# Kernel optimization log

Hardware: AMD Instinct MI355X
Metric: run time of the kernel (lower is better)

Reference implementation:

```python
import jax, jax.numpy as jnp
import numpy as np

B, T, C, H = 2, 2048, 1024, 16
HD = C // H  # head dim = 64


def setup_inputs() -> dict:
    key = jax.random.key(0)
    ks = jax.random.split(key, 5)
    s = 0.02
    return {
        "x": jax.random.normal(ks[0], (B, T, C), dtype=jnp.float32),
        "w_attn": jax.random.normal(ks[1], (C, 3 * C), dtype=jnp.float32) * s,
        "b_attn": jnp.zeros((3 * C,), dtype=jnp.float32),
        "w_proj": jax.random.normal(ks[2], (C, C), dtype=jnp.float32) * s,
        "b_proj": jnp.zeros((C,), dtype=jnp.float32),
    }


def reference(x, w_attn, b_attn, w_proj, b_proj):
    Bc, Tc, Cc = x.shape
    qkv = x @ w_attn + b_attn                      # [B,T,3C]
    q, k, v = jnp.split(qkv, 3, axis=2)            # each [B,T,C]
    # [B,T,C] -> [B,H,T,HD]
    def heads(t):
        return t.reshape(Bc, Tc, H, HD).transpose(0, 2, 1, 3)
    q, k, v = heads(q), heads(k), heads(v)
    scale = 1.0 / jnp.sqrt(jnp.asarray(HD, dtype=x.dtype))
    att = jnp.einsum("bhqd,bhkd->bhqk", q, k) * scale   # [B,H,T,T]
    causal = jnp.tril(jnp.ones((Tc, Tc), dtype=bool))
    att = jnp.where(causal, att, jnp.asarray(-jnp.inf, dtype=att.dtype))
    att = jax.nn.softmax(att, axis=-1)
    y = jnp.einsum("bhqk,bhkd->bhqd", att, v)            # [B,H,T,HD]
    y = y.transpose(0, 2, 1, 3).reshape(Bc, Tc, Cc)      # [B,T,C]
    return y @ w_proj + b_proj
```

## Files before the change

### kernel.cpp

```cpp
#include <hip/hip_runtime.h>
#include <stdint.h>


typedef short bf16x8 __attribute__((ext_vector_type(8)));
typedef float f32x4 __attribute__((ext_vector_type(4)));

__device__ inline unsigned short f2bf(float f) {
  union { float f; uint32_t u; } v; v.f = f;
  uint32_t u = v.u;
  u += 0x7FFFu + ((u >> 16) & 1u);
  return (unsigned short)(u >> 16);
}

__device__ inline unsigned pkbf(float a, float b) {
  unsigned r;
  asm("v_cvt_pk_bf16_f32 %0, %1, %2" : "=v"(r) : "v"(a), "v"(b));
  return r;
}

__device__ inline float exp2_fast(float x) {
#if __has_builtin(__builtin_amdgcn_exp2f)
  return __builtin_amdgcn_exp2f(x);
#else
  float r; asm("v_exp_f32 %0, %1" : "=v"(r) : "v"(x)); return r;
#endif
}

__device__ inline void load_lds16(const unsigned short* g, unsigned short* l) {
  __builtin_amdgcn_global_load_lds(
      (const __attribute__((address_space(1))) unsigned int*)(const void*)g,
      (__attribute__((address_space(3))) unsigned int*)(void*)l, 16, 0, 0);
}

__global__ __launch_bounds__(256) void cast_bf16_kernel(
    const float* __restrict__ in, unsigned short* __restrict__ out, int n4) {
  int i = blockIdx.x * 256 + threadIdx.x;
  if (i >= n4) return;
  float4 f = reinterpret_cast<const float4*>(in)[i];
  ushort4 o;
  o.x = f2bf(f.x); o.y = f2bf(f.y); o.z = f2bf(f.z); o.w = f2bf(f.w);
  reinterpret_cast<ushort4*>(out)[i] = o;
}

__global__ void transpose_cast_kernel(
    const float* __restrict__ in, unsigned short* __restrict__ out, int R, int Cn) {
  __shared__ float tile[32][33];
  int bx = blockIdx.x * 32, by = blockIdx.y * 32;
  int tx = threadIdx.x, ty = threadIdx.y;
  #pragma unroll
  for (int i = 0; i < 32; i += 8)
    tile[ty + i][tx] = in[(size_t)(by + ty + i) * Cn + bx + tx];
  __syncthreads();
  #pragma unroll
  for (int i = 0; i < 32; i += 8)
    out[(size_t)(bx + ty + i) * R + by + tx] = f2bf(tile[tx][ty + i]);
}

template<int BM, int BN>
__global__ __launch_bounds__(256) void gemm_bt_kernel(
    const unsigned short* __restrict__ A,
    const unsigned short* __restrict__ Bt,
    const float* __restrict__ bias,
    void* __restrict__ outp,
    unsigned short* __restrict__ vtp,
    int M, int N, int K, int mode) {
  constexpr int MT = BM / 32, NT = BN / 32;
  constexpr int RPWA = BM / 4, RPWB = BN / 4;
  constexpr int NJA = RPWA / 16, NJB = RPWB / 16;
  __shared__ unsigned short As[2][BM * 32];
  __shared__ unsigned short Bs[2][BN * 32];
  const int t = threadIdx.x;
  const int wave = t >> 6, lane = t & 63;
  const int L = lane & 15, quad = lane >> 4;
  const int wm = (wave >> 1) * (BM / 2), wn = (wave & 1) * (BN / 2);
  const int m0 = blockIdx.y * BM, n0 = blockIdx.x * BN;

  const int drow = lane >> 2;
  const int dch  = (lane & 3) ^ ((drow >> 1) & 3);
  const int foff = ((quad ^ ((L >> 1) & 3)) * 8);

  const unsigned short* Ab = A  + (size_t)(m0 + wave * RPWA + drow) * K + dch * 8;
  const unsigned short* Bb = Bt + (size_t)(n0 + wave * RPWB + drow) * K + dch * 8;

  f32x4 acc[MT][NT] = {};
  const int NK = K >> 5;

  #pragma unroll
  for (int j = 0; j < NJA; ++j)
    load_lds16(Ab + (size_t)j * 16 * K, &As[0][(wave * RPWA + j * 16) * 32]);
  #pragma unroll
  for (int j = 0; j < NJB; ++j)
    load_lds16(Bb + (size_t)j * 16 * K, &Bs[0][(wave * RPWB + j * 16) * 32]);

  int buf = 0;
  for (int kt = 0; kt < NK; ++kt) {
    asm volatile("" ::: "memory");
    __builtin_amdgcn_s_waitcnt(0x0F70);
    __builtin_amdgcn_s_barrier();
    asm volatile("" ::: "memory");

    if (kt + 1 < NK) {
      #pragma unroll
      for (int j = 0; j < NJA; ++j)
        load_lds16(Ab + (size_t)j * 16 * K + (kt + 1) * 32,
                   &As[buf ^ 1][(wave * RPWA + j * 16) * 32]);
      #pragma unroll
      for (int j = 0; j < NJB; ++j)
        load_lds16(Bb + (size_t)j * 16 * K + (kt + 1) * 32,
                   &Bs[buf ^ 1][(wave * RPWB + j * 16) * 32]);
    }

    bf16x8 af[MT], bf[NT];
    #pragma unroll
    for (int mt = 0; mt < MT; ++mt)
      af[mt] = *reinterpret_cast<const bf16x8*>(&As[buf][(wm + mt * 16 + L) * 32 + foff]);
    #pragma unroll
    for (int nt = 0; nt < NT; ++nt)
      bf[nt] = *reinterpret_cast<const bf16x8*>(&Bs[buf][(wn + nt * 16 + L) * 32 + foff]);
    __builtin_amdgcn_s_setprio(1);
    #pragma unroll
    for (int mt = 0; mt < MT; ++mt)
      #pragma unroll
      for (int nt = 0; nt < NT; ++nt)
        acc[mt][nt] = __builtin_amdgcn_mfma_f32_16x16x32_bf16(af[mt], bf[nt], acc[mt][nt], 0, 0, 0);
    __builtin_amdgcn_s_setprio(0);
    buf ^= 1;
  }

  if (mode == 0) {
    float* out = (float*)outp;
    #pragma unroll
    for (int mt = 0; mt < MT; ++mt)
      #pragma unroll
      for (int nt = 0; nt < NT; ++nt) {
        int col = n0 + wn + nt * 16 + L;
        float b = bias[col];
        #pragma unroll
        for (int r = 0; r < 4; ++r) {
          int row = m0 + wm + mt * 16 + quad * 4 + r;
          out[(size_t)row * N + col] = acc[mt][nt][r] + b;
        }
      }
  } else {
    unsigned short* qkv = (unsigned short*)outp;
    #pragma unroll
    for (int mt = 0; mt < MT; ++mt)
      #pragma unroll
      for (int nt = 0; nt < NT; ++nt) {
        int col = n0 + wn + nt * 16 + L;
        int sel = col >> 10, cc = col & 1023;
        int h = cc >> 6, d = cc & 63;
        float b = bias[col];
        float sc = (sel == 0) ? 0.18033688011112042f : 1.0f;
        #pragma unroll
        for (int r = 0; r < 4; ++r) {
          int row = m0 + wm + mt * 16 + quad * 4 + r;
          int bb = row >> 11, tt = row & 2047;
          float val = (acc[mt][nt][r] + b) * sc;
          if (sel == 2) {
            vtp[((size_t)(bb * 16 + h) * 64 + d) * 2048 + tt] = f2bf(val);
          } else {
            qkv[(((size_t)sel * 32 + (size_t)(bb * 16 + h)) * 2048 + tt) * 64 + d] = f2bf(val);
          }
        }
      }
  }
}

__global__ __launch_bounds__(256) void attn_kernel(
    const unsigned short* __restrict__ qkv,
    const unsigned short* __restrict__ vt,
    unsigned short* __restrict__ y) {
  __shared__ unsigned short Ks[3][64 * 64];
  __shared__ unsigned short Vs[3][64 * 64];
  __shared__ unsigned short Ps[4][32][72];

  const int t = threadIdx.x;
  const int wave = t >> 6, lane = t & 63;
  const int L = lane & 15, quad = lane >> 4;
  const int b = blockIdx.x;
  const int bh = (b & 7) * 4 + ((b >> 3) & 3);
  const int pi = b >> 5;
  const int tA = pi, tB = 31 - pi;
  const int rowA0 = tA * 64 + wave * 16;
  const int rowB0 = tB * 64 + wave * 16;
  const int ntiles = tB + 1;

  const unsigned short* qb  = qkv + ((size_t)bh * 2048) * 64;
  const unsigned short* kb  = qkv + ((size_t)(32 + bh) * 2048) * 64;
  const unsigned short* vtb = vt + (size_t)bh * 64 * 2048;

  const int drow = lane >> 3;
  const int dch  = (lane & 7) ^ drow;
  const int fo0 = ((quad ^ (L & 7)) * 8);
  const int fo1 = (((quad + 4) ^ (L & 7)) * 8);

  bf16x8 qfA[2], qfB[2];
  #pragma unroll
  for (int h = 0; h < 2; ++h) {
    qfA[h] = *reinterpret_cast<const bf16x8*>(qb + (size_t)(rowA0 + L) * 64 + h * 32 + quad * 8);
    qfB[h] = *reinterpret_cast<const bf16x8*>(qb + (size_t)(rowB0 + L) * 64 + h * 32 + quad * 8);
  }

  f32x4 oA[4] = {}, oB[4] = {};
  float rsA = 0.f, rsB = 0.f;

  {
    #pragma unroll
    for (int j = 0; j < 2; ++j) {
      int r0 = wave * 16 + j * 8;
      load_lds16(kb  + (size_t)(0 + r0 + drow) * 64 + dch * 8, &Ks[0][r0 * 64]);
      load_lds16(vtb + (size_t)(r0 + drow) * 2048 + 0 + dch * 8, &Vs[0][r0 * 64]);
    }
  }

  int buf = 0;
  for (int kt = 0; kt < ntiles; ++kt) {
    const int nkt = (kt + 1 < ntiles) ? kt + 1 : ntiles - 1;
    const int nbuf = (buf == 2) ? 0 : buf + 1;
    {
      const int kg = nkt * 64;
      #pragma unroll
      for (int j = 0; j < 2; ++j) {
        int r0 = wave * 16 + j * 8;
        load_lds16(kb  + (size_t)(kg + r0 + drow) * 64 + dch * 8, &Ks[nbuf][r0 * 64]);
        load_lds16(vtb + (size_t)(r0 + drow) * 2048 + kg + dch * 8, &Vs[nbuf][r0 * 64]);
      }
    }
    asm volatile("" ::: "memory");
    __builtin_amdgcn_s_waitcnt(0x0F74);
    __builtin_amdgcn_s_barrier();
    asm volatile("" ::: "memory");

    const bool actA = (kt <= tA);

    bf16x8 kf[4][2];
    #pragma unroll
    for (int nt = 0; nt < 4; ++nt) {
      kf[nt][0] = *reinterpret_cast<const bf16x8*>(&Ks[buf][(nt * 16 + L) * 64 + fo0]);
      kf[nt][1] = *reinterpret_cast<const bf16x8*>(&Ks[buf][(nt * 16 + L) * 64 + fo1]);
    }

    f32x4 sB[4] = {};
    __builtin_amdgcn_s_setprio(1);
    #pragma unroll
    for (int nt = 0; nt < 4; ++nt) {
      sB[nt] = __builtin_amdgcn_mfma_f32_16x16x32_bf16(kf[nt][0], qfB[0], sB[nt], 0, 0, 0);
      sB[nt] = __builtin_amdgcn_mfma_f32_16x16x32_bf16(kf[nt][1], qfB[1], sB[nt], 0, 0, 0);
    }
    __builtin_amdgcn_s_setprio(0);
    if (kt == tB) {
      #pragma unroll
      for (int nt = 0; nt < 4; ++nt) {
        int key0 = kt * 64 + nt * 16 + quad * 4;
        int qr = rowB0 + L;
        #pragma unroll
        for (int r = 0; r < 4; ++r)
          if (key0 + r > qr) sB[nt][r] = -3.0e38f;
      }
    }
    #pragma unroll
    for (int nt = 0; nt < 4; ++nt) {
      float p0 = exp2_fast(sB[nt][0]), p1 = exp2_fast(sB[nt][1]);
      float p2 = exp2_fast(sB[nt][2]), p3 = exp2_fast(sB[nt][3]);
      rsB += (p0 + p1) + (p2 + p3);
      uint2 pk;
      pk.x = pkbf(p0, p1);
      pk.y = pkbf(p2, p3);
      *reinterpret_cast<uint2*>(&Ps[wave][16 + L][nt * 16 + quad * 4]) = pk;
    }

    if (actA) {
      f32x4 sA[4] = {};
      __builtin_amdgcn_s_setprio(1);
      #pragma unroll
      for (int nt = 0; nt < 4; ++nt) {
        sA[nt] = __builtin_amdgcn_mfma_f32_16x16x32_bf16(kf[nt][0], qfA[0], sA[nt], 0, 0, 0);
        sA[nt] = __builtin_amdgcn_mfma_f32_16x16x32_bf16(kf[nt][1], qfA[1], sA[nt], 0, 0, 0);
      }
      __builtin_amdgcn_s_setprio(0);
      if (kt == tA) {
        #pragma unroll
        for (int nt = 0; nt < 4; ++nt) {
          int key0 = kt * 64 + nt * 16 + quad * 4;
          int qr = rowA0 + L;
          #pragma unroll
          for (int r = 0; r < 4; ++r)
            if (key0 + r > qr) sA[nt][r] = -3.0e38f;
        }
      }
      #pragma unroll
      for (int nt = 0; nt < 4; ++nt) {
        float p0 = exp2_fast(sA[nt][0]), p1 = exp2_fast(sA[nt][1]);
        float p2 = exp2_fast(sA[nt][2]), p3 = exp2_fast(sA[nt][3]);
        rsA += (p0 + p1) + (p2 + p3);
        uint2 pk;
        pk.x = pkbf(p0, p1);
        pk.y = pkbf(p2, p3);
        *reinterpret_cast<uint2*>(&Ps[wave][L][nt * 16 + quad * 4]) = pk;
      }
    }

    bf16x8 vf[4][2];
    #pragma unroll
    for (int nt = 0; nt < 4; ++nt) {
      vf[nt][0] = *reinterpret_cast<const bf16x8*>(&Vs[buf][(nt * 16 + L) * 64 + fo0]);
      vf[nt][1] = *reinterpret_cast<const bf16x8*>(&Vs[buf][(nt * 16 + L) * 64 + fo1]);
    }
    bf16x8 pb0 = *reinterpret_cast<const bf16x8*>(&Ps[wave][16 + L][quad * 8]);
    bf16x8 pb1 = *reinterpret_cast<const bf16x8*>(&Ps[wave][16 + L][32 + quad * 8]);
    __builtin_amdgcn_s_setprio(1);
    #pragma unroll
    for (int nt = 0; nt < 4; ++nt) {
      oB[nt] = __builtin_amdgcn_mfma_f32_16x16x32_bf16(pb0, vf[nt][0], oB[nt], 0, 0, 0);
      oB[nt] = __builtin_amdgcn_mfma_f32_16x16x32_bf16(pb1, vf[nt][1], oB[nt], 0, 0, 0);
    }
    __builtin_amdgcn_s_setprio(0);
    if (actA) {
      bf16x8 pa0 = *reinterpret_cast<const bf16x8*>(&Ps[wave][L][quad * 8]);
      bf16x8 pa1 = *reinterpret_cast<const bf16x8*>(&Ps[wave][L][32 + quad * 8]);
      __builtin_amdgcn_s_setprio(1);
      #pragma unroll
      for (int nt = 0; nt < 4; ++nt) {
        oA[nt] = __builtin_amdgcn_mfma_f32_16x16x32_bf16(pa0, vf[nt][0], oA[nt], 0, 0, 0);
        oA[nt] = __builtin_amdgcn_mfma_f32_16x16x32_bf16(pa1, vf[nt][1], oA[nt], 0, 0, 0);
      }
      __builtin_amdgcn_s_setprio(0);
    }
    buf = nbuf;
  }

  float a = rsA; a += __shfl_xor(a, 16, 64); a += __shfl_xor(a, 32, 64);
  float b2 = rsB; b2 += __shfl_xor(b2, 16, 64); b2 += __shfl_xor(b2, 32, 64);
  float invA[4], invB[4];
  #pragma unroll
  for (int r = 0; r < 4; ++r) {
    invA[r] = 1.0f / __shfl(a, quad * 4 + r, 64);
    invB[r] = 1.0f / __shfl(b2, quad * 4 + r, 64);
  }
  const int bb = bh >> 4, hh = bh & 15;
  #pragma unroll
  for (int nt = 0; nt < 4; ++nt)
    #pragma unroll
    for (int r = 0; r < 4; ++r) {
      int rA = rowA0 + quad * 4 + r;
      int rB = rowB0 + quad * 4 + r;
      int col = hh * 64 + nt * 16 + L;
      y[((size_t)bb * 2048 + rA) * 1024 + col] = f2bf(oA[nt][r] * invA[r]);
      y[((size_t)bb * 2048 + rB) * 1024 + col] = f2bf(oB[nt][r] * invB[r]);
    }
  __builtin_amdgcn_s_waitcnt(0);
}

extern "C" void kernel_launch(void* const* d_in, const int* in_sizes, int n_in,
                              void* d_out, int out_size, void* d_ws, size_t ws_size,
                              hipStream_t stream) {
  const float* x      = (const float*)d_in[0];
  const float* w_attn = (const float*)d_in[1];
  const float* b_attn = (const float*)d_in[2];
  const float* w_proj = (const float*)d_in[3];
  const float* b_proj = (const float*)d_in[4];
  float* out = (float*)d_out;

  unsigned short* ws = (unsigned short*)d_ws;
  unsigned short* xb     = ws;
  unsigned short* wattnT = xb + 4194304;
  unsigned short* wprojT = wattnT + 3145728;
  unsigned short* qkv    = wprojT + 1048576;
  unsigned short* yb     = qkv + 12582912;
  unsigned short* vt     = yb + 4194304;

  cast_bf16_kernel<<<4096, 256, 0, stream>>>(x, xb, 1048576);
  transpose_cast_kernel<<<dim3(96, 32), dim3(32, 8), 0, stream>>>(w_attn, wattnT, 1024, 3072);
  transpose_cast_kernel<<<dim3(32, 32), dim3(32, 8), 0, stream>>>(w_proj, wprojT, 1024, 1024);

  gemm_bt_kernel<128, 128><<<dim3(24, 32), 256, 0, stream>>>(xb, wattnT, b_attn, qkv, vt, 4096, 3072, 1024, 1);
  attn_kernel<<<dim3(512), 256, 0, stream>>>(qkv, vt, yb);
  gemm_bt_kernel<64, 64><<<dim3(16, 64), 256, 0, stream>>>(yb, wprojT, b_proj, out, nullptr, 4096, 1024, 1024, 0);
}
```

Before: 181.1 us.

## Fuse prep kernels into one launch and use K=64 tiles in QKV GEMM

Merges the input cast and the two weight transpose-casts into a single prep kernel that dispatches by block index, removing two kernel launches. The QKV projection GEMM moves to a dedicated kernel with a 64-wide K tile, an 8-chunk XOR swizzle, and two MFMA sub-steps per barrier, halving the number of barriers and load rounds. This doubles LDS use per block (64KB), which may reduce occupancy. The output projection keeps the old template, minus its mode switch.

```diff
diff --git a/kernel.cpp b/kernel.cpp
--- a/kernel.cpp
+++ b/kernel.cpp
@@ -32,21 +32,32 @@
       (__attribute__((address_space(3))) unsigned int*)(void*)l, 16, 0, 0);
 }
 
-__global__ __launch_bounds__(256) void cast_bf16_kernel(
-    const float* __restrict__ in, unsigned short* __restrict__ out, int n4) {
-  int i = blockIdx.x * 256 + threadIdx.x;
-  if (i >= n4) return;
-  float4 f = reinterpret_cast<const float4*>(in)[i];
-  ushort4 o;
-  o.x = f2bf(f.x); o.y = f2bf(f.y); o.z = f2bf(f.z); o.w = f2bf(f.w);
-  reinterpret_cast<ushort4*>(out)[i] = o;
-}
-
-__global__ void transpose_cast_kernel(
-    const float* __restrict__ in, unsigned short* __restrict__ out, int R, int Cn) {
+__global__ __launch_bounds__(256) void prep_kernel(
+    const float* __restrict__ x, const float* __restrict__ w_attn,
+    const float* __restrict__ w_proj,
+    unsigned short* __restrict__ xb, unsigned short* __restrict__ wattnT,
+    unsigned short* __restrict__ wprojT) {
   __shared__ float tile[32][33];
-  int bx = blockIdx.x * 32, by = blockIdx.y * 32;
-  int tx = threadIdx.x, ty = threadIdx.y;
+  const int b = blockIdx.x, t = threadIdx.x;
+  if (b < 4096) {
+    int i = b * 256 + t;
+    float4 f = reinterpret_cast<const float4*>(x)[i];
+    ushort4 o;
+    o.x = f2bf(f.x); o.y = f2bf(f.y); o.z = f2bf(f.z); o.w = f2bf(f.w);
+    reinterpret_cast<ushort4*>(xb)[i] = o;
+    return;
+  }
+  const float* in; unsigned short* out; int R, Cn, bx, by;
+  if (b < 7168) {
+    int bb = b - 4096;
+    in = w_attn; out = wattnT; R = 1024; Cn = 3072;
+    bx = (bb % 96) * 32; by = (bb / 96) * 32;
+  } else {
+    int bb = b - 7168;
+    in = w_proj; out = wprojT; R = 1024; Cn = 1024;
+    bx = (bb % 32) * 32; by = (bb / 32) * 32;
+  }
+  const int tx = t & 31, ty = t >> 5;
   #pragma unroll
   for (int i = 0; i < 32; i += 8)
     tile[ty + i][tx] = in[(size_t)(by + ty + i) * Cn + bx + tx];
@@ -56,72 +67,81 @@
     out[(size_t)(bx + ty + i) * R + by + tx] = f2bf(tile[tx][ty + i]);
 }
 
-template<int BM, int BN>
-__global__ __launch_bounds__(256) void gemm_bt_kernel(
+__global__ __launch_bounds__(256) void gemm_bt64_kernel(
     const unsigned short* __restrict__ A,
     const unsigned short* __restrict__ Bt,
     const float* __restrict__ bias,
     void* __restrict__ outp,
     unsigned short* __restrict__ vtp,
     int M, int N, int K, int mode) {
-  constexpr int MT = BM / 32, NT = BN / 32;
-  constexpr int RPWA = BM / 4, RPWB = BN / 4;
-  constexpr int NJA = RPWA / 16, NJB = RPWB / 16;
-  __shared__ unsigned short As[2][BM * 32];
-  __shared__ unsigned short Bs[2][BN * 32];
+  __shared__ unsigned short As[2][128 * 64];
+  __shared__ unsigned short Bs[2][128 * 64];
   const int t = threadIdx.x;
   const int wave = t >> 6, lane = t & 63;
   const int L = lane & 15, quad = lane >> 4;
-  const int wm = (wave >> 1) * (BM / 2), wn = (wave & 1) * (BN / 2);
-  const int m0 = blockIdx.y * BM, n0 = blockIdx.x * BN;
-
-  const int drow = lane >> 2;
-  const int dch  = (lane & 3) ^ ((drow >> 1) & 3);
-  const int foff = ((quad ^ ((L >> 1) & 3)) * 8);
-
-  const unsigned short* Ab = A  + (size_t)(m0 + wave * RPWA + drow) * K + dch * 8;
-  const unsigned short* Bb = Bt + (size_t)(n0 + wave * RPWB + drow) * K + dch * 8;
-
-  f32x4 acc[MT][NT] = {};
-  const int NK = K >> 5;
-
-  #pragma unroll
-  for (int j = 0; j < NJA; ++j)
-    load_lds16(Ab + (size_t)j * 16 * K, &As[0][(wave * RPWA + j * 16) * 32]);
-  #pragma unroll
-  for (int j = 0; j < NJB; ++j)
-    load_lds16(Bb + (size_t)j * 16 * K, &Bs[0][(wave * RPWB + j * 16) * 32]);
+  const int wm = (wave >> 1) * 64, wn = (wave & 1) * 64;
+  const int m0 = blockIdx.y * 128, n0 = blockIdx.x * 128;
+
+  const int drow = lane >> 3;
+  const int dch  = (lane & 7) ^ drow;
+  const int fo0 = ((quad ^ (L & 7)) * 8);
+  const int fo1 = (((quad + 4) ^ (L & 7)) * 8);
+
+  const unsigned short* Ab = A  + (size_t)(m0 + wave * 32 + drow) * K + dch * 8;
+  const unsigned short* Bb = Bt + (size_t)(n0 + wave * 32 + drow) * K + dch * 8;
+
+  f32x4 acc[4][4] = {};
+  const int NK2 = K >> 6;
+
+  #pragma unroll
+  for (int j = 0; j < 4; ++j) {
+    int r0 = wave * 32 + j * 8;
+    load_lds16(Ab + (size_t)j * 8 * K, &As[0][r0 * 64]);
+    load_lds16(Bb + (size_t)j * 8 * K, &Bs[0][r0 * 64]);
+  }
 
   int buf = 0;
-  for (int kt = 0; kt < NK; ++kt) {
+  for (int kt = 0; kt < NK2; ++kt) {
     asm volatile("" ::: "memory");
     __builtin_amdgcn_s_waitcnt(0x0F70);
     __builtin_amdgcn_s_barrier();
     asm volatile("" ::: "memory");
 
-    if (kt + 1 < NK) {
-      #pragma unroll
-      for (int j = 0; j < NJA; ++j)
-        load_lds16(Ab + (size_t)j * 16 * K + (kt + 1) * 32,
-                   &As[buf ^ 1][(wave * RPWA + j * 16) * 32]);
-      #pragma unroll
-      for (int j = 0; j < NJB; ++j)
-        load_lds16(Bb + (size_t)j * 16 * K + (kt + 1) * 32,
-                   &Bs[buf ^ 1][(wave * RPWB + j * 16) * 32]);
-    }
-
-    bf16x8 af[MT], bf[NT];
-    #pragma unroll
-    for (int mt = 0; mt < MT; ++mt)
-      af[mt] = *reinterpret_cast<const bf16x8*>(&As[buf][(wm + mt * 16 + L) * 32 + foff]);
-    #pragma unroll
-    for (int nt = 0; nt < NT; ++nt)
-      bf[nt] = *reinterpret_cast<const bf16x8*>(&Bs[buf][(wn + nt * 16 + L) * 32 + foff]);
+    if (kt + 1 < NK2) {
+      #pragma unroll
+      for (int j = 0; j < 4; ++j) {
+        int r0 = wave * 32 + j * 8;
+        load_lds16(Ab + (size_t)j * 8 * K + (size_t)(kt + 1) * 64, &As[buf ^ 1][r0 * 64]);
+        load_lds16(Bb + (size_t)j * 8 * K + (size_t)(kt + 1) * 64, &Bs[buf ^ 1][r0 * 64]);
+      }
+    }
+
+    bf16x8 af[4], bf[4];
+    #pragma unroll
+    for (int mt = 0; mt < 4; ++mt)
+      af[mt] = *reinterpret_cast<const bf16x8*>(&As[buf][(wm + mt * 16 + L) * 64 + fo0]);
+    #pragma unroll
+    for (int nt = 0; nt < 4; ++nt)
+      bf[nt] = *reinterpret_cast<const bf16x8*>(&Bs[buf][(wn + nt * 16 + L) * 64 + fo0]);
     __builtin_amdgcn_s_setprio(1);
     #pragma unroll
-    for (int mt = 0; mt < MT; ++mt)
-      #pragma unroll
-      for (int nt = 0; nt < NT; ++nt)
+    for (int mt = 0; mt < 4; ++mt)
+      #pragma unroll
+      for (int nt = 0; nt < 4; ++nt)
+        acc[mt][nt] = __builtin_amdgcn_mfma_f32_16x16x32_bf16(af[mt], bf[nt], acc[mt][nt], 0, 0, 0);
+    __builtin_amdgcn_s_setprio(0);
+
+    #pragma unroll
+    for (int mt = 0; mt < 4; ++mt)
+      af[mt] = *reinterpret_cast<const bf16x8*>(&As[buf][(wm + mt * 16 + L) * 64 + fo1]);
+    #pragma unroll
+    for (int nt = 0; nt < 4; ++nt)
+      bf[nt] = *reinterpret_cast<const bf16x8*>(&Bs[buf][(wn + nt * 16 + L) * 64 + fo1]);
+    __builtin_amdgcn_s_setprio(1);
+    #pragma unroll
+    for (int mt = 0; mt < 4; ++mt)
+      #pragma unroll
+      for (int nt = 0; nt < 4; ++nt)
         acc[mt][nt] = __builtin_amdgcn_mfma_f32_16x16x32_bf16(af[mt], bf[nt], acc[mt][nt], 0, 0, 0);
     __builtin_amdgcn_s_setprio(0);
     buf ^= 1;
@@ -130,9 +150,9 @@
   if (mode == 0) {
     float* out = (float*)outp;
     #pragma unroll
-    for (int mt = 0; mt < MT; ++mt)
-      #pragma unroll
-      for (int nt = 0; nt < NT; ++nt) {
+    for (int mt = 0; mt < 4; ++mt)
+      #pragma unroll
+      for (int nt = 0; nt < 4; ++nt) {
         int col = n0 + wn + nt * 16 + L;
         float b = bias[col];
         #pragma unroll
@@ -144,9 +164,9 @@
   } else {
     unsigned short* qkv = (unsigned short*)outp;
     #pragma unroll
-    for (int mt = 0; mt < MT; ++mt)
-      #pragma unroll
-      for (int nt = 0; nt < NT; ++nt) {
+    for (int mt = 0; mt < 4; ++mt)
+      #pragma unroll
+      for (int nt = 0; nt < 4; ++nt) {
         int col = n0 + wn + nt * 16 + L;
         int sel = col >> 10, cc = col & 1023;
         int h = cc >> 6, d = cc & 63;
@@ -167,6 +187,90 @@
   }
 }
 
+template<int BM, int BN>
+__global__ __launch_bounds__(256) void gemm_bt_kernel(
+    const unsigned short* __restrict__ A,
+    const unsigned short* __restrict__ Bt,
+    const float* __restrict__ bias,
+    float* __restrict__ out,
+    int M, int N, int K) {
+  constexpr int MT = BM / 32, NT = BN / 32;
+  constexpr int RPWA = BM / 4, RPWB = BN / 4;
+  constexpr int NJA = RPWA / 16, NJB = RPWB / 16;
+  __shared__ unsigned short As[2][BM * 32];
+  __shared__ unsigned short Bs[2][BN * 32];
+  const int t = threadIdx.x;
+  const int wave = t >> 6, lane = t & 63;
+  const int L = lane & 15, quad = lane >> 4;
+  const int wm = (wave >> 1) * (BM / 2), wn = (wave & 1) * (BN / 2);
+  const int m0 = blockIdx.y * BM, n0 = blockIdx.x * BN;
+
+  const int drow = lane >> 2;
+  const int dch  = (lane & 3) ^ ((drow >> 1) & 3);
+  const int foff = ((quad ^ ((L >> 1) & 3)) * 8);
+
+  const unsigned short* Ab = A  + (size_t)(m0 + wave * RPWA + drow) * K + dch * 8;
+  const unsigned short* Bb = Bt + (size_t)(n0 + wave * RPWB + drow) * K + dch * 8;
+
+  f32x4 acc[MT][NT] = {};
+  const int NK = K >> 5;
+
+  #pragma unroll
+  for (int j = 0; j < NJA; ++j)
+    load_lds16(Ab + (size_t)j * 16 * K, &As[0][(wave * RPWA + j * 16) * 32]);
+  #pragma unroll
+  for (int j = 0; j < NJB; ++j)
+    load_lds16(Bb + (size_t)j * 16 * K, &Bs[0][(wave * RPWB + j * 16) * 32]);
+
+  int buf = 0;
+  for (int kt = 0; kt < NK; ++kt) {
+    asm volatile("" ::: "memory");
+    __builtin_amdgcn_s_waitcnt(0x0F70);
+    __builtin_amdgcn_s_barrier();
+    asm volatile("" ::: "memory");
+
+    if (kt + 1 < NK) {
+      #pragma unroll
+      for (int j = 0; j < NJA; ++j)
+        load_lds16(Ab + (size_t)j * 16 * K + (kt + 1) * 32,
+                   &As[buf ^ 1][(wave * RPWA + j * 16) * 32]);
+      #pragma unroll
+      for (int j = 0; j < NJB; ++j)
+        load_lds16(Bb + (size_t)j * 16 * K + (kt + 1) * 32,
+                   &Bs[buf ^ 1][(wave * RPWB + j * 16) * 32]);
+    }
+
+    bf16x8 af[MT], bf[NT];
+    #pragma unroll
+    for (int mt = 0; mt < MT; ++mt)
+      af[mt] = *reinterpret_cast<const bf16x8*>(&As[buf][(wm + mt * 16 + L) * 32 + foff]);
+    #pragma unroll
+    for (int nt = 0; nt < NT; ++nt)
+      bf[nt] = *reinterpret_cast<const bf16x8*>(&Bs[buf][(wn + nt * 16 + L) * 32 + foff]);
+    __builtin_amdgcn_s_setprio(1);
+    #pragma unroll
+    for (int mt = 0; mt < MT; ++mt)
+      #pragma unroll
+      for (int nt = 0; nt < NT; ++nt)
+        acc[mt][nt] = __builtin_amdgcn_mfma_f32_16x16x32_bf16(af[mt], bf[nt], acc[mt][nt], 0, 0, 0);
+    __builtin_amdgcn_s_setprio(0);
+    buf ^= 1;
+  }
+
+  #pragma unroll
+  for (int mt = 0; mt < MT; ++mt)
+    #pragma unroll
+    for (int nt = 0; nt < NT; ++nt) {
+      int col = n0 + wn + nt * 16 + L;
+      float b = bias[col];
+      #pragma unroll
+      for (int r = 0; r < 4; ++r) {
+        int row = m0 + wm + mt * 16 + quad * 4 + r;
+        out[(size_t)row * N + col] = acc[mt][nt][r] + b;
+      }
+    }
+}
+
 __global__ __launch_bounds__(256) void attn_kernel(
     const unsigned short* __restrict__ qkv,
     const unsigned short* __restrict__ vt,
@@ -370,11 +474,9 @@
   unsigned short* yb     = qkv + 12582912;
   unsigned short* vt     = yb + 4194304;
 
-  cast_bf16_kernel<<<4096, 256, 0, stream>>>(x, xb, 1048576);
-  transpose_cast_kernel<<<dim3(96, 32), dim3(32, 8), 0, stream>>>(w_attn, wattnT, 1024, 3072);
-  transpose_cast_kernel<<<dim3(32, 32), dim3(32, 8), 0, stream>>>(w_proj, wprojT, 1024, 1024);
-
-  gemm_bt_kernel<128, 128><<<dim3(24, 32), 256, 0, stream>>>(xb, wattnT, b_attn, qkv, vt, 4096, 3072, 1024, 1);
+  prep_kernel<<<8192, 256, 0, stream>>>(x, w_attn, w_proj, xb, wattnT, wprojT);
+
+  gemm_bt64_kernel<<<dim3(24, 32), 256, 0, stream>>>(xb, wattnT, b_attn, qkv, vt, 4096, 3072, 1024, 1);
   attn_kernel<<<dim3(512), 256, 0, stream>>>(qkv, vt, yb);
-  gemm_bt_kernel<64, 64><<<dim3(16, 64), 256, 0, stream>>>(yb, wprojT, b_proj, out, nullptr, 4096, 1024, 1024, 0);
-}
+  gemm_bt_kernel<64, 64><<<dim3(16, 64), 256, 0, stream>>>(yb, wprojT, b_proj, out, 4096, 1024, 1024);
+}
```

After: 190.9 us. 1.05x slower.
